# Optimization experiments

Hardware: AMD Instinct MI355X
Metric: run time of the kernel (lower is better)

Reference implementation:

```python
import jax, jax.numpy as jnp
import numpy as np
from jax import lax

C = 8          # bargs.channel
S = 1024       # bargs.test_sidelen
SIGMA = 1.0    # edge_sigma
KS = int(6 * SIGMA + 1)   # 7
PAD = KS // 2             # 3
BW = S // 6               # border_width
LAM, MU, TH = 5.0, 5.0, 1e-4


def _edge_kernel():
    coords = jnp.arange(KS, dtype=jnp.float32) - (KS - 1.0) / 2.0
    g1 = jnp.exp(-coords ** 2 / (2.0 * SIGMA ** 2))
    g1 = g1 / g1.sum()
    g2 = jnp.outer(g1, g1)
    return jnp.broadcast_to(g2, (C, 1, KS, KS))  # depthwise OIHW


def _alpha():
    # max applicable loop index among {row-dist, col-dist}; interior stays 1.
    r = jnp.arange(S)
    g = jnp.where(r < BW, r, jnp.where(S - 1 - r < BW, S - 1 - r, -1))  # [S]
    m = jnp.maximum(g[:, None], g[None, :])                              # [S,S]
    a = jnp.where(m >= 0, m.astype(jnp.float32) / BW, 1.0)
    return a[None, None]  # [1,1,S,S] broadcasts over channels


def _grad_spectrum():
    gv = jnp.array([[-1., -2., -1.], [0., 0., 0.], [1., 2., 1.]], jnp.float32)
    gh = gv.T
    gvf = jnp.fft.fft2(gv, s=(S, S))
    ghf = jnp.fft.fft2(gh, s=(S, S))
    return (jnp.abs(gvf) ** 2 + jnp.abs(ghf) ** 2).astype(jnp.float32)  # real


def _edge_blur(img, kernel, alpha):
    blurred = lax.conv_general_dilated(
        img, kernel, window_strides=(1, 1), padding=[(PAD, PAD), (PAD, PAD)],
        feature_group_count=C, dimension_numbers=('NCHW', 'OIHW', 'NCHW'))
    return alpha * img + (1.0 - alpha) * blurred


def setup_inputs() -> dict:
    key = jax.random.key(0)
    k1, k2 = jax.random.split(key)
    lms = jax.random.uniform(k1, (1, C, S, S), dtype=jnp.float32)
    fuse = jax.random.uniform(k2, (1, C, S, S), dtype=jnp.float32)
    return {"lms": lms, "fuse": fuse}


def reference(lms, fuse):
    kernel = _edge_kernel()
    alpha = _alpha()
    grad = _grad_spectrum()

    lms_fft = jnp.fft.fft2(_edge_blur(lms, kernel, alpha))
    fuse_fft = jnp.fft.fft2(_edge_blur(fuse, kernel, alpha))

    denom = jnp.abs(fuse_fft) ** 2 + LAM + MU * grad      # real [1,C,S,S]
    numer = jnp.conj(fuse_fft) * lms_fft
    psf = jnp.fft.fftshift(jnp.real(jnp.fft.ifft2(numer / denom)), axes=(-2, -1))
    psf = jnp.where(psf < TH, 0.0, psf)                   # [1,C,S,S]

    def crop(p):  # p: [S,S]
        row, col = jnp.unravel_index(jnp.argmax(p), p.shape)
        patch = lax.dynamic_slice(p, (row - 20, col - 20), (41, 41))
        return patch / jnp.sum(patch)

    psf_l = jax.vmap(crop)(psf[0])        # [C,41,41]
    return psf_l[:, None]                 # [C,1,41,41]
```

## Files before the change

kernel.cpp:

```cpp
#include <hip/hip_runtime.h>
#include <math.h>

#define SS 1024
#define NC 8
#define BWD 170
#define THRESH 1e-4f

typedef unsigned long long ull;

__device__ __forceinline__ float2 cmul(float2 a, float2 b) {
    return make_float2(a.x * b.x - a.y * b.y, a.x * b.y + a.y * b.x);
}

#define XS(a) ((a) ^ (((a) >> 4) & 15))

__device__ __forceinline__ int cmap(int kx) {
    if (kx == 0) return 0;
    if (kx == 512) return 1;
    return (kx < 512) ? (kx << 1) : (((1024 - kx) << 1) | 1);
}

template <int DIR>
__device__ __forceinline__ void bfly4(const float2 v[4], float2 r[4]) {
    float2 a = v[0], b = v[1], c = v[2], d = v[3];
    float2 apc = make_float2(a.x + c.x, a.y + c.y);
    float2 amc = make_float2(a.x - c.x, a.y - c.y);
    float2 bpd = make_float2(b.x + d.x, b.y + d.y);
    float2 jb  = make_float2(-(b.y - d.y), b.x - d.x);
    r[0] = make_float2(apc.x + bpd.x, apc.y + bpd.y);
    r[2] = make_float2(apc.x - bpd.x, apc.y - bpd.y);
    if (DIR == -1) {
        r[1] = make_float2(amc.x - jb.x, amc.y - jb.y);
        r[3] = make_float2(amc.x + jb.x, amc.y + jb.y);
    } else {
        r[1] = make_float2(amc.x + jb.x, amc.y + jb.y);
        r[3] = make_float2(amc.x - jb.x, amc.y - jb.y);
    }
}

template <int DIR>
__device__ __forceinline__ void fft1024_reg(float2 v[4], float2* A, float2* B,
                                            int tid, bool sb) {
    float2* dst = A;
    float2* alt = B;
    #pragma unroll
    for (int t = 0; t < 4; ++t) {
        int s = 1 << (2 * t);
        int k = tid & ~(s - 1);
        float2 r[4];
        bfly4<DIR>(v, r);
        float rev = (float)k * (1.0f / 1024.0f);
        float2 w1 = make_float2(__builtin_amdgcn_cosf(rev),
                                (float)DIR * __builtin_amdgcn_sinf(rev));
        float2 w2 = cmul(w1, w1);
        float2 w3 = cmul(w2, w1);
        int base = tid + 3 * k;
        dst[XS(base)]         = r[0];
        dst[XS(base + s)]     = cmul(r[1], w1);
        dst[XS(base + 2 * s)] = cmul(r[2], w2);
        dst[XS(base + 3 * s)] = cmul(r[3], w3);
        __syncthreads();
        v[0] = dst[XS(tid)];
        v[1] = dst[XS(tid + 256)];
        v[2] = dst[XS(tid + 512)];
        v[3] = dst[XS(tid + 768)];
        if (sb) __syncthreads();
        float2* tmp = dst; dst = alt; alt = tmp;
    }
    float2 r[4];
    bfly4<DIR>(v, r);
    v[0] = r[0]; v[1] = r[1]; v[2] = r[2]; v[3] = r[3];
}

#define PIDX(r) ((r) + ((r) >> 5))

__global__ __launch_bounds__(256) void blur_fft_kernel(
        const float* __restrict__ lms, const float* __restrict__ fuse,
        float2* __restrict__ Zf) {
    __shared__ float2 bufA[1024];
    __shared__ float2 smemB2[1068];
    float* rowl = (float*)smemB2;
    float* rowf = rowl + 1068;
    int tid = threadIdx.x;
    int g = blockIdx.x;
    int c = g >> 10;
    int y = (g & 7) * 128 + ((g >> 3) & 127);
    const float* L = lms + ((size_t)c << 20);
    const float* F = fuse + ((size_t)c << 20);
    int x0 = tid << 2;

    double e1 = exp(-0.5), e2 = exp(-2.0), e3 = exp(-4.5);
    double sm = 1.0 + 2.0 * (e1 + e2 + e3);
    float w[7] = { (float)(e3 / sm), (float)(e2 / sm), (float)(e1 / sm),
                   (float)(1.0 / sm),
                   (float)(e1 / sm), (float)(e2 / sm), (float)(e3 / sm) };

    bool rowInt = (y >= BWD) && (y <= SS - 1 - BWD);
    bool skipLoads = rowInt && (tid >= 45) && (tid <= 210);
    bool doH = !rowInt || (tid <= 43) || (tid >= 212);

    float4 cl, cf;
    if (skipLoads) {
        cl = *(const float4*)&L[((size_t)y << 10) + x0];
        cf = *(const float4*)&F[((size_t)y << 10) + x0];
    } else {
        float4 lv[7], fv[7];
        #pragma unroll
        for (int r = 0; r < 7; ++r) {
            int gy = y - 3 + r;
            if (gy >= 0 && gy < SS) {
                lv[r] = *(const float4*)&L[((size_t)gy << 10) + x0];
                fv[r] = *(const float4*)&F[((size_t)gy << 10) + x0];
            } else {
                lv[r] = make_float4(0.f, 0.f, 0.f, 0.f);
                fv[r] = make_float4(0.f, 0.f, 0.f, 0.f);
            }
        }
        cl = lv[3]; cf = fv[3];
        #pragma unroll
        for (int j = 0; j < 4; ++j) {
            float a = 0.f, b = 0.f;
            #pragma unroll
            for (int r = 0; r < 7; ++r) {
                a += w[r] * (&lv[r].x)[j];
                b += w[r] * (&fv[r].x)[j];
            }
            rowl[PIDX(3 + x0 + j)] = a;
            rowf[PIDX(3 + x0 + j)] = b;
        }
    }
    if (tid < 3) {
        rowl[PIDX(tid)] = 0.f; rowf[PIDX(tid)] = 0.f;
        rowl[PIDX(1027 + tid)] = 0.f; rowf[PIDX(1027 + tid)] = 0.f;
    }
    __syncthreads();

    float bl[4] = {0.f, 0.f, 0.f, 0.f}, bf[4] = {0.f, 0.f, 0.f, 0.f};
    if (doH) {
        #pragma unroll
        for (int k = 0; k < 4; ++k) {
            float a = 0.f, b = 0.f;
            #pragma unroll
            for (int j = 0; j < 7; ++j) {
                a += w[j] * rowl[PIDX(x0 + k + j)];
                b += w[j] * rowf[PIDX(x0 + k + j)];
            }
            bl[k] = a; bf[k] = b;
        }
    }
    int gyv = (y < BWD) ? y : ((SS - 1 - y) < BWD ? (SS - 1 - y) : -1);
    #pragma unroll
    for (int k = 0; k < 4; ++k) {
        int x = x0 + k;
        int gx = (x < BWD) ? x : ((SS - 1 - x) < BWD ? (SS - 1 - x) : -1);
        int m = gyv > gx ? gyv : gx;
        float a = (m >= 0) ? (float)m / (float)BWD : 1.0f;
        bufA[XS(x)] = make_float2(a * (&cl.x)[k] + (1.0f - a) * bl[k],
                                  a * (&cf.x)[k] + (1.0f - a) * bf[k]);
    }
    __syncthreads();

    float2 v[4];
    #pragma unroll
    for (int m = 0; m < 4; ++m) v[m] = bufA[XS(tid + (m << 8))];
    fft1024_reg<-1>(v, smemB2, bufA, tid, false);

    float2* Zrow = Zf + (((size_t)c << 20) + ((size_t)y << 10));
    #pragma unroll
    for (int r = 0; r < 4; ++r) Zrow[cmap(tid + (r << 8))] = v[r];
}

__global__ __launch_bounds__(256) void fft2_wiener_kernel(
        const float2* __restrict__ Z, float2* __restrict__ Wb) {
    __shared__ float2 resbuf[4][1024];
    int tid = threadIdx.x;
    int p = blockIdx.x >> 9;
    int b0 = blockIdx.x & 511;
    int i = ((b0 & 7) << 6) | (b0 >> 3);
    int rows[2];
    rows[0] = (i == 0) ? 0 : i;
    rows[1] = (i == 0) ? 512 : 1024 - i;
    bool selfp = (i == 0);
    int slot = (i == 0) ? 0 : (i << 1);

    const float2* Zp0 = Z + ((size_t)(2 * p) << 20);
    const float2* Zp1 = Z + ((size_t)(2 * p + 1) << 20);
    float4 q0[4], q1[4];
    #pragma unroll
    for (int m = 0; m < 4; ++m)
        q0[m] = *(const float4*)&Zp0[((size_t)(tid + (m << 8)) << 10) + slot];
    #pragma unroll
    for (int m = 0; m < 4; ++m)
        q1[m] = *(const float4*)&Zp1[((size_t)(tid + (m << 8)) << 10) + slot];

    float2 v[4];
    #pragma unroll
    for (int m = 0; m < 4; ++m) v[m] = make_float2(q0[m].x, q0[m].y);
    fft1024_reg<-1>(v, resbuf[2], resbuf[0], tid, false);
    #pragma unroll
    for (int r = 0; r < 4; ++r) resbuf[0][XS(tid + (r << 8))] = v[r];
    #pragma unroll
    for (int m = 0; m < 4; ++m) v[m] = make_float2(q0[m].z, q0[m].w);
    fft1024_reg<-1>(v, resbuf[1], resbuf[2], tid, false);
    #pragma unroll
    for (int r = 0; r < 4; ++r) resbuf[2][XS(tid + (r << 8))] = v[r];
    #pragma unroll
    for (int m = 0; m < 4; ++m) v[m] = make_float2(q1[m].x, q1[m].y);
    fft1024_reg<-1>(v, resbuf[3], resbuf[1], tid, false);
    #pragma unroll
    for (int r = 0; r < 4; ++r) resbuf[1][XS(tid + (r << 8))] = v[r];
    #pragma unroll
    for (int m = 0; m < 4; ++m) v[m] = make_float2(q1[m].z, q1[m].w);
    fft1024_reg<-1>(v, resbuf[3], resbuf[3], tid, true);
    #pragma unroll
    for (int r = 0; r < 4; ++r) resbuf[3][XS(tid + (r << 8))] = v[r];
    __syncthreads();

    float2 gout[2][4];
    #pragma unroll
    for (int o = 0; o < 2; ++o) {
        int u = rows[o];
        int po = selfp ? o : (1 - o);
        float cu = __builtin_amdgcn_cosf((float)u * (1.0f / 1024.0f));
        float c2u = 2.0f * cu * cu - 1.0f;
        float hu = 2.0f + 2.0f * cu;
        #pragma unroll
        for (int j = 0; j < 4; ++j) {
            int vv = tid + (j << 8);
            int vn = (1024 - vv) & 1023;
            float cv = __builtin_amdgcn_cosf((float)vv * (1.0f / 1024.0f));
            float c2v = 2.0f * cv * cv - 1.0f;
            float hv = 2.0f + 2.0f * cv;
            float grad = (2.0f - 2.0f * c2v) * hu * hu +
                         (2.0f - 2.0f * c2u) * hv * hv;
            float regs = 5.0f + 5.0f * grad;
            float G0x, G0y, G1x, G1y;
            #pragma unroll
            for (int c = 0; c < 2; ++c) {
                float2 a = resbuf[o * 2 + c][XS(vv)];
                float2 b = resbuf[po * 2 + c][XS(vn)];
                float Lx = 0.5f * (a.x + b.x), Ly = 0.5f * (a.y - b.y);
                float Fx = 0.5f * (a.y + b.y), Fy = -0.5f * (a.x - b.x);
                float inv = 1.0f / (Fx * Fx + Fy * Fy + regs);
                float nx = (Fx * Lx + Fy * Ly) * inv;
                float ny = (Fx * Ly - Fy * Lx) * inv;
                if (c == 0) { G0x = nx; G0y = ny; } else { G1x = nx; G1y = ny; }
            }
            gout[o][j] = make_float2(G0x - G1y, G0y + G1x);
        }
    }
    __syncthreads();

    const float isc = 1.0f / 1024.0f;
    #pragma unroll
    for (int o = 0; o < 2; ++o) {
        float2 iv[4];
        #pragma unroll
        for (int j = 0; j < 4; ++j) iv[j] = gout[o][j];
        fft1024_reg<1>(iv, resbuf[1 + 2 * o], resbuf[2 * o], tid, false);
        float2* go = Wb + (((size_t)p << 20) + ((size_t)rows[o] << 10));
        #pragma unroll
        for (int r = 0; r < 4; ++r)
            go[tid + (r << 8)] = make_float2(iv[r].x * isc, iv[r].y * isc);
    }
}

__global__ __launch_bounds__(256) void ifft_final_kernel(
        const float2* __restrict__ Wd, float* __restrict__ psf,
        ull* __restrict__ bm) {
    __shared__ float2 bufA[1024];
    __shared__ float2 bufB[1024];
    int tid = threadIdx.x;
    int wv = tid >> 6;
    int p = blockIdx.x >> 9;
    int b0 = blockIdx.x & 511;
    int y0 = (((b0 & 7) << 6) | (b0 >> 3)) << 1;
    const float2* g = Wd + (((size_t)p << 20) + y0);
    float4 q[4];
    #pragma unroll
    for (int m = 0; m < 4; ++m)
        q[m] = *(const float4*)&g[(size_t)(tid + (m << 8)) << 10];

    const float sc = 1.0f / 1024.0f;
    #pragma unroll
    for (int half = 0; half < 2; ++half) {
        int y = y0 + half;
        float2 v[4];
        #pragma unroll
        for (int m = 0; m < 4; ++m)
            v[m] = half ? make_float2(q[m].z, q[m].w)
                        : make_float2(q[m].x, q[m].y);
        fft1024_reg<1>(v, bufA, bufB, tid, false);

        int oy = (y + 512) & 1023;
        float* p0 = psf + (((size_t)(2 * p) << 20) + ((size_t)oy << 10));
        float* p1 = p0 + (1u << 20);
        ull e0 = 0, e1 = 0;
        #pragma unroll
        for (int r = 0; r < 4; ++r) {
            int k = tid + (r << 8);
            float re = v[r].x * sc; re = (re < THRESH) ? 0.0f : re;
            float im = v[r].y * sc; im = (im < THRESH) ? 0.0f : im;
            int ox = (k + 512) & 1023;
            p0[ox] = re;
            p1[ox] = im;
            unsigned int idx = ((unsigned int)oy << 10) | (unsigned int)ox;
            ull c0 = ((ull)__float_as_uint(re) << 32) | (ull)(0xFFFFFFFFu - idx);
            ull c1 = ((ull)__float_as_uint(im) << 32) | (ull)(0xFFFFFFFFu - idx);
            e0 = c0 > e0 ? c0 : e0;
            e1 = c1 > e1 ? c1 : e1;
        }
        #pragma unroll
        for (int off = 32; off > 0; off >>= 1) {
            ull o0 = __shfl_down(e0, off);
            ull o1 = __shfl_down(e1, off);
            e0 = o0 > e0 ? o0 : e0;
            e1 = o1 > e1 ? o1 : e1;
        }
        if ((tid & 63) == 0) {
            bm[((size_t)(2 * p) << 12) + (y << 2) + wv] = e0;
            bm[((size_t)(2 * p + 1) << 12) + (y << 2) + wv] = e1;
        }
    }
}

__global__ __launch_bounds__(256) void crop_kernel(
        const float* __restrict__ psf, const ull* __restrict__ bm,
        float* __restrict__ out) {
    int c = blockIdx.x;
    __shared__ ull rmax[256];
    __shared__ float red[256];
    int tid = threadIdx.x;
    ull e = 0;
    for (int i = tid; i < 4096; i += 256) {
        ull v = bm[((size_t)c << 12) + i];
        e = v > e ? v : e;
    }
    rmax[tid] = e;
    __syncthreads();
    for (int s2 = 128; s2 > 0; s2 >>= 1) {
        if (tid < s2) { ull a = rmax[tid], b = rmax[tid + s2]; rmax[tid] = a > b ? a : b; }
        __syncthreads();
    }
    unsigned int bidx = 0xFFFFFFFFu - (unsigned int)(rmax[0] & 0xFFFFFFFFull);
    int row = (int)(bidx >> 10), col = (int)(bidx & 1023);
    int r0 = row - 20; if (r0 < 0) r0 = 0; if (r0 > SS - 41) r0 = SS - 41;
    int c0 = col - 20; if (c0 < 0) c0 = 0; if (c0 > SS - 41) c0 = SS - 41;
    const float* p = psf + ((size_t)c << 20);
    float local = 0.0f;
    for (int i = tid; i < 1681; i += 256) {
        int rr = i / 41, cc = i - rr * 41;
        local += p[(size_t)(r0 + rr) * SS + c0 + cc];
    }
    red[tid] = local;
    __syncthreads();
    for (int s2 = 128; s2 > 0; s2 >>= 1) {
        if (tid < s2) red[tid] += red[tid + s2];
        __syncthreads();
    }
    float inv = 1.0f / red[0];
    for (int i = tid; i < 1681; i += 256) {
        int rr = i / 41, cc = i - rr * 41;
        out[c * 1681 + i] = p[(size_t)(r0 + rr) * SS + c0 + cc] * inv;
    }
}

extern "C" void kernel_launch(void* const* d_in, const int* in_sizes, int n_in,
                              void* d_out, int out_size, void* d_ws,
                              size_t ws_size, hipStream_t stream) {
    const float* lms = (const float*)d_in[0];
    const float* fuse = (const float*)d_in[1];
    char* ws = (char*)d_ws;
    float2* Zf = (float2*)ws;
    float2* Wb = (float2*)(ws + ((size_t)64 << 20));
    float* psf = (float*)ws;
    ull* bm = (ull*)(ws + ((size_t)33 << 20));
    float* outp = (float*)d_out;

    blur_fft_kernel<<<8192, 256, 0, stream>>>(lms, fuse, Zf);
    fft2_wiener_kernel<<<2048, 256, 0, stream>>>(Zf, Wb);
    ifft_final_kernel<<<2048, 256, 0, stream>>>(Wb, psf, bm);
    crop_kernel<<<8, 256, 0, stream>>>(psf, bm, outp);
}
```

Before: 190.4 us.

## Run independent FFTs concurrently with two 256-thread groups per block

The column-FFT/Wiener kernel and the final inverse-FFT kernel now launch 512 threads per block. Two 256-thread groups work on different FFTs in parallel instead of one group doing them one after another. This cuts the serial chain of FFT stages and barriers per block and raises thread-level parallelism. In exchange, each block-wide __syncthreads now spans both groups, and the launch bound of (512, 8) may force more register pressure or spilling.

```diff
diff --git a/kernel.cpp b/kernel.cpp
--- a/kernel.cpp
+++ b/kernel.cpp
@@ -40,13 +40,13 @@
 
 template <int DIR>
 __device__ __forceinline__ void fft1024_reg(float2 v[4], float2* A, float2* B,
-                                            int tid, bool sb) {
+                                            int t, bool sb) {
     float2* dst = A;
     float2* alt = B;
     #pragma unroll
-    for (int t = 0; t < 4; ++t) {
-        int s = 1 << (2 * t);
-        int k = tid & ~(s - 1);
+    for (int st = 0; st < 4; ++st) {
+        int s = 1 << (2 * st);
+        int k = t & ~(s - 1);
         float2 r[4];
         bfly4<DIR>(v, r);
         float rev = (float)k * (1.0f / 1024.0f);
@@ -54,16 +54,16 @@
                                 (float)DIR * __builtin_amdgcn_sinf(rev));
         float2 w2 = cmul(w1, w1);
         float2 w3 = cmul(w2, w1);
-        int base = tid + 3 * k;
+        int base = t + 3 * k;
         dst[XS(base)]         = r[0];
         dst[XS(base + s)]     = cmul(r[1], w1);
         dst[XS(base + 2 * s)] = cmul(r[2], w2);
         dst[XS(base + 3 * s)] = cmul(r[3], w3);
         __syncthreads();
-        v[0] = dst[XS(tid)];
-        v[1] = dst[XS(tid + 256)];
-        v[2] = dst[XS(tid + 512)];
-        v[3] = dst[XS(tid + 768)];
+        v[0] = dst[XS(t)];
+        v[1] = dst[XS(t + 256)];
+        v[2] = dst[XS(t + 512)];
+        v[3] = dst[XS(t + 768)];
         if (sb) __syncthreads();
         float2* tmp = dst; dst = alt; alt = tmp;
     }
@@ -170,10 +170,12 @@
     for (int r = 0; r < 4; ++r) Zrow[cmap(tid + (r << 8))] = v[r];
 }
 
-__global__ __launch_bounds__(256) void fft2_wiener_kernel(
+__global__ __launch_bounds__(512, 8) void fft2_wiener_kernel(
         const float2* __restrict__ Z, float2* __restrict__ Wb) {
     __shared__ float2 resbuf[4][1024];
     int tid = threadIdx.x;
+    int grp = tid >> 8;
+    int t = tid & 255;
     int p = blockIdx.x >> 9;
     int b0 = blockIdx.x & 511;
     int i = ((b0 & 7) << 6) | (b0 >> 3);
@@ -183,42 +185,28 @@
     bool selfp = (i == 0);
     int slot = (i == 0) ? 0 : (i << 1);
 
-    const float2* Zp0 = Z + ((size_t)(2 * p) << 20);
-    const float2* Zp1 = Z + ((size_t)(2 * p + 1) << 20);
-    float4 q0[4], q1[4];
+    const float2* Zp = Z + ((size_t)(2 * p + grp) << 20);
+    float4 q[4];
     #pragma unroll
     for (int m = 0; m < 4; ++m)
-        q0[m] = *(const float4*)&Zp0[((size_t)(tid + (m << 8)) << 10) + slot];
-    #pragma unroll
-    for (int m = 0; m < 4; ++m)
-        q1[m] = *(const float4*)&Zp1[((size_t)(tid + (m << 8)) << 10) + slot];
+        q[m] = *(const float4*)&Zp[((size_t)(t + (m << 8)) << 10) + slot];
 
     float2 v[4];
     #pragma unroll
-    for (int m = 0; m < 4; ++m) v[m] = make_float2(q0[m].x, q0[m].y);
-    fft1024_reg<-1>(v, resbuf[2], resbuf[0], tid, false);
-    #pragma unroll
-    for (int r = 0; r < 4; ++r) resbuf[0][XS(tid + (r << 8))] = v[r];
-    #pragma unroll
-    for (int m = 0; m < 4; ++m) v[m] = make_float2(q0[m].z, q0[m].w);
-    fft1024_reg<-1>(v, resbuf[1], resbuf[2], tid, false);
-    #pragma unroll
-    for (int r = 0; r < 4; ++r) resbuf[2][XS(tid + (r << 8))] = v[r];
-    #pragma unroll
-    for (int m = 0; m < 4; ++m) v[m] = make_float2(q1[m].x, q1[m].y);
-    fft1024_reg<-1>(v, resbuf[3], resbuf[1], tid, false);
-    #pragma unroll
-    for (int r = 0; r < 4; ++r) resbuf[1][XS(tid + (r << 8))] = v[r];
-    #pragma unroll
-    for (int m = 0; m < 4; ++m) v[m] = make_float2(q1[m].z, q1[m].w);
-    fft1024_reg<-1>(v, resbuf[3], resbuf[3], tid, true);
-    #pragma unroll
-    for (int r = 0; r < 4; ++r) resbuf[3][XS(tid + (r << 8))] = v[r];
-    __syncthreads();
-
-    float2 gout[2][4];
-    #pragma unroll
-    for (int o = 0; o < 2; ++o) {
+    for (int m = 0; m < 4; ++m) v[m] = make_float2(q[m].x, q[m].y);
+    fft1024_reg<-1>(v, resbuf[2 + grp], resbuf[grp], t, false);
+    #pragma unroll
+    for (int r = 0; r < 4; ++r) resbuf[grp][XS(t + (r << 8))] = v[r];
+    #pragma unroll
+    for (int m = 0; m < 4; ++m) v[m] = make_float2(q[m].z, q[m].w);
+    fft1024_reg<-1>(v, resbuf[2 + grp], resbuf[2 + grp], t, true);
+    #pragma unroll
+    for (int r = 0; r < 4; ++r) resbuf[2 + grp][XS(t + (r << 8))] = v[r];
+    __syncthreads();
+
+    float2 gi[4];
+    {
+        int o = grp;
         int u = rows[o];
         int po = selfp ? o : (1 - o);
         float cu = __builtin_amdgcn_cosf((float)u * (1.0f / 1024.0f));
@@ -226,7 +214,7 @@
         float hu = 2.0f + 2.0f * cu;
         #pragma unroll
         for (int j = 0; j < 4; ++j) {
-            int vv = tid + (j << 8);
+            int vv = t + (j << 8);
             int vn = (1024 - vv) & 1023;
             float cv = __builtin_amdgcn_cosf((float)vv * (1.0f / 1024.0f));
             float c2v = 2.0f * cv * cv - 1.0f;
@@ -246,81 +234,73 @@
                 float ny = (Fx * Ly - Fy * Lx) * inv;
                 if (c == 0) { G0x = nx; G0y = ny; } else { G1x = nx; G1y = ny; }
             }
-            gout[o][j] = make_float2(G0x - G1y, G0y + G1x);
+            gi[j] = make_float2(G0x - G1y, G0y + G1x);
         }
     }
     __syncthreads();
 
+    fft1024_reg<1>(gi, resbuf[grp], resbuf[2 + grp], t, false);
     const float isc = 1.0f / 1024.0f;
-    #pragma unroll
-    for (int o = 0; o < 2; ++o) {
-        float2 iv[4];
-        #pragma unroll
-        for (int j = 0; j < 4; ++j) iv[j] = gout[o][j];
-        fft1024_reg<1>(iv, resbuf[1 + 2 * o], resbuf[2 * o], tid, false);
-        float2* go = Wb + (((size_t)p << 20) + ((size_t)rows[o] << 10));
-        #pragma unroll
-        for (int r = 0; r < 4; ++r)
-            go[tid + (r << 8)] = make_float2(iv[r].x * isc, iv[r].y * isc);
-    }
-}
-
-__global__ __launch_bounds__(256) void ifft_final_kernel(
+    float2* go = Wb + (((size_t)p << 20) + ((size_t)rows[grp] << 10));
+    #pragma unroll
+    for (int r = 0; r < 4; ++r)
+        go[t + (r << 8)] = make_float2(gi[r].x * isc, gi[r].y * isc);
+}
+
+__global__ __launch_bounds__(512, 8) void ifft_final_kernel(
         const float2* __restrict__ Wd, float* __restrict__ psf,
         ull* __restrict__ bm) {
-    __shared__ float2 bufA[1024];
-    __shared__ float2 bufB[1024];
+    __shared__ float2 buf[2][2][1024];
     int tid = threadIdx.x;
-    int wv = tid >> 6;
+    int grp = tid >> 8;
+    int t = tid & 255;
+    int wvloc = (tid >> 6) & 3;
     int p = blockIdx.x >> 9;
     int b0 = blockIdx.x & 511;
     int y0 = (((b0 & 7) << 6) | (b0 >> 3)) << 1;
+    int y = y0 + grp;
     const float2* g = Wd + (((size_t)p << 20) + y0);
     float4 q[4];
     #pragma unroll
     for (int m = 0; m < 4; ++m)
-        q[m] = *(const float4*)&g[(size_t)(tid + (m << 8)) << 10];
+        q[m] = *(const float4*)&g[(size_t)(t + (m << 8)) << 10];
+
+    float2 v[4];
+    #pragma unroll
+    for (int m = 0; m < 4; ++m)
+        v[m] = grp ? make_float2(q[m].z, q[m].w)
+                   : make_float2(q[m].x, q[m].y);
+    fft1024_reg<1>(v, buf[grp][0], buf[grp][1], t, false);
 
     const float sc = 1.0f / 1024.0f;
-    #pragma unroll
-    for (int half = 0; half < 2; ++half) {
-        int y = y0 + half;
-        float2 v[4];
-        #pragma unroll
-        for (int m = 0; m < 4; ++m)
-            v[m] = half ? make_float2(q[m].z, q[m].w)
-                        : make_float2(q[m].x, q[m].y);
-        fft1024_reg<1>(v, bufA, bufB, tid, false);
-
-        int oy = (y + 512) & 1023;
-        float* p0 = psf + (((size_t)(2 * p) << 20) + ((size_t)oy << 10));
-        float* p1 = p0 + (1u << 20);
-        ull e0 = 0, e1 = 0;
-        #pragma unroll
-        for (int r = 0; r < 4; ++r) {
-            int k = tid + (r << 8);
-            float re = v[r].x * sc; re = (re < THRESH) ? 0.0f : re;
-            float im = v[r].y * sc; im = (im < THRESH) ? 0.0f : im;
-            int ox = (k + 512) & 1023;
-            p0[ox] = re;
-            p1[ox] = im;
-            unsigned int idx = ((unsigned int)oy << 10) | (unsigned int)ox;
-            ull c0 = ((ull)__float_as_uint(re) << 32) | (ull)(0xFFFFFFFFu - idx);
-            ull c1 = ((ull)__float_as_uint(im) << 32) | (ull)(0xFFFFFFFFu - idx);
-            e0 = c0 > e0 ? c0 : e0;
-            e1 = c1 > e1 ? c1 : e1;
-        }
-        #pragma unroll
-        for (int off = 32; off > 0; off >>= 1) {
-            ull o0 = __shfl_down(e0, off);
-            ull o1 = __shfl_down(e1, off);
-            e0 = o0 > e0 ? o0 : e0;
-            e1 = o1 > e1 ? o1 : e1;
-        }
-        if ((tid & 63) == 0) {
-            bm[((size_t)(2 * p) << 12) + (y << 2) + wv] = e0;
-            bm[((size_t)(2 * p + 1) << 12) + (y << 2) + wv] = e1;
-        }
+    int oy = (y + 512) & 1023;
+    float* p0 = psf + (((size_t)(2 * p) << 20) + ((size_t)oy << 10));
+    float* p1 = p0 + (1u << 20);
+    ull e0 = 0, e1 = 0;
+    #pragma unroll
+    for (int r = 0; r < 4; ++r) {
+        int k = t + (r << 8);
+        float re = v[r].x * sc; re = (re < THRESH) ? 0.0f : re;
+        float im = v[r].y * sc; im = (im < THRESH) ? 0.0f : im;
+        int ox = (k + 512) & 1023;
+        p0[ox] = re;
+        p1[ox] = im;
+        unsigned int idx = ((unsigned int)oy << 10) | (unsigned int)ox;
+        ull c0 = ((ull)__float_as_uint(re) << 32) | (ull)(0xFFFFFFFFu - idx);
+        ull c1 = ((ull)__float_as_uint(im) << 32) | (ull)(0xFFFFFFFFu - idx);
+        e0 = c0 > e0 ? c0 : e0;
+        e1 = c1 > e1 ? c1 : e1;
+    }
+    #pragma unroll
+    for (int off = 32; off > 0; off >>= 1) {
+        ull o0 = __shfl_down(e0, off);
+        ull o1 = __shfl_down(e1, off);
+        e0 = o0 > e0 ? o0 : e0;
+        e1 = o1 > e1 ? o1 : e1;
+    }
+    if ((tid & 63) == 0) {
+        bm[((size_t)(2 * p) << 12) + (y << 2) + wvloc] = e0;
+        bm[((size_t)(2 * p + 1) << 12) + (y << 2) + wvloc] = e1;
     }
 }
 
@@ -378,7 +358,7 @@
     float* outp = (float*)d_out;
 
     blur_fft_kernel<<<8192, 256, 0, stream>>>(lms, fuse, Zf);
-    fft2_wiener_kernel<<<2048, 256, 0, stream>>>(Zf, Wb);
-    ifft_final_kernel<<<2048, 256, 0, stream>>>(Wb, psf, bm);
+    fft2_wiener_kernel<<<2048, 512, 0, stream>>>(Zf, Wb);
+    ifft_final_kernel<<<2048, 512, 0, stream>>>(Wb, psf, bm);
     crop_kernel<<<8, 256, 0, stream>>>(psf, bm, outp);
 }
```

After: 228.4 us. 20.0% more time.
